# Performance work log

Measured on AMD Instinct MI355X. Metric: run time of the kernel, lower is better.

Reference implementation:

```python
import jax, jax.numpy as jnp
import numpy as np

B, T, U, D, INNER, VOCAB = 4, 256, 64, 512, 512, 2048

def setup_inputs() -> dict:
    key = jax.random.key(0)
    ks = jax.random.split(key, 6)
    return {
        "enc_state": jax.random.normal(ks[0], (B, T, D), jnp.float32),
        "dec_state": jax.random.normal(ks[1], (B, U, D), jnp.float32),
        "W1": jax.random.normal(ks[2], (2 * D, INNER), jnp.float32) * 0.02,
        "b1": jax.random.normal(ks[3], (INNER,), jnp.float32) * 0.02,
        "W2": jax.random.normal(ks[4], (INNER, VOCAB), jnp.float32) * 0.02,
        "b2": jax.random.normal(ks[5], (VOCAB,), jnp.float32) * 0.02,
    }

def reference(enc_state, dec_state, W1, b1, W2, b2):
    # concat([enc, dec]) @ W1 == enc @ W1[:D] + dec @ W1[D:]  (same math,
    # avoids materializing the [B,T,U,2D] repeat+cat tensor)
    d = enc_state.shape[-1]
    We, Wd = W1[:d], W1[d:]
    enc_proj = jnp.einsum('btd,dk->btk', enc_state, We)           # [B,T,INNER]
    dec_proj = jnp.einsum('bud,dk->buk', dec_state, Wd)           # [B,U,INNER]
    hidden = jnp.tanh(enc_proj[:, :, None, :] + dec_proj[:, None, :, :] + b1)  # [B,T,U,INNER]
    logits = jnp.einsum('btuk,kv->btuv', hidden, W2) + b2          # [B,T,U,VOCAB]
    return logits
```

## Files before the change

kernel.cpp:

```cpp
#include <hip/hip_runtime.h>
#include <hip/hip_bf16.h>

#define B_  4
#define T_  256
#define U_  64
#define D_  512
#define INNER_ 512
#define VOCAB_ 2048

typedef __attribute__((ext_vector_type(8))) short short8;
typedef __attribute__((ext_vector_type(4))) float f32x4;

__global__ __launch_bounds__(256) void prep_kernel(
    const float* __restrict__ enc, const float* __restrict__ dec,
    const float* __restrict__ W1, const float* __restrict__ b1,
    const float* __restrict__ W2,
    float* __restrict__ encP, float* __restrict__ decPb,
    __hip_bfloat16* __restrict__ W2T) {
  __shared__ float ldsbuf[16 * D_];
  int tid = threadIdx.x;
  int bidx = blockIdx.x;

  if (bidx < 320) {
    int ct = bidx & 3;
    int rt = bidx >> 2;
    const float* src; float* dst; int kOff; int addB1; int rowBase;
    if (rt < 64) { src = enc; dst = encP; kOff = 0; addB1 = 0; rowBase = rt * 16; }
    else { src = dec; dst = decPb; kOff = D_; addB1 = 1; rowBase = (rt - 64) * 16; }

    float (*As)[D_] = (float(*)[D_])ldsbuf;
    const float4* s4 = (const float4*)(src + (size_t)rowBase * D_);
    float4* a4 = (float4*)(&As[0][0]);
#pragma unroll
    for (int i = 0; i < 8; i++) a4[tid + 256 * i] = s4[tid + 256 * i];
    __syncthreads();

    int colQ = (tid & 31) * 4;
    int col = ct * 128 + colQ;
    int r0 = (tid >> 5) * 2;
    float a00=0,a01=0,a02=0,a03=0, a10=0,a11=0,a12=0,a13=0;
    const float* Wp = W1 + (size_t)kOff * INNER_ + col;
#pragma unroll 4
    for (int k = 0; k < D_; k++) {
      float4 w = *(const float4*)(Wp + (size_t)k * INNER_);
      float e0 = As[r0][k], e1 = As[r0 + 1][k];
      a00 += e0 * w.x; a01 += e0 * w.y; a02 += e0 * w.z; a03 += e0 * w.w;
      a10 += e1 * w.x; a11 += e1 * w.y; a12 += e1 * w.z; a13 += e1 * w.w;
    }
    float4 bb = {0,0,0,0};
    if (addB1) bb = *(const float4*)(b1 + col);
    float4 o0 = {a00 + bb.x, a01 + bb.y, a02 + bb.z, a03 + bb.w};
    float4 o1 = {a10 + bb.x, a11 + bb.y, a12 + bb.z, a13 + bb.w};
    *(float4*)(dst + (size_t)(rowBase + r0) * INNER_ + col) = o0;
    *(float4*)(dst + (size_t)(rowBase + r0 + 1) * INNER_ + col) = o1;
  } else {
    int b = bidx - 320;
    int vBase = (b & 63) * 32;
    int kBase = (b >> 6) * 32;
    float (*tile)[33] = (float(*)[33])ldsbuf;
    int tx = tid & 31, ty = tid >> 5;
#pragma unroll
    for (int i = 0; i < 32; i += 8)
      tile[ty + i][tx] = W2[(size_t)(kBase + ty + i) * VOCAB_ + vBase + tx];
    __syncthreads();
#pragma unroll
    for (int i = 0; i < 32; i += 8)
      W2T[(size_t)(vBase + ty + i) * INNER_ + kBase + tx] = __float2bfloat16(tile[tx][ty + i]);
  }
}

__global__ __launch_bounds__(256) void hidden_kernel(
    const float* __restrict__ encP, const float* __restrict__ decPb,
    __hip_bfloat16* __restrict__ H) {
  int gid = blockIdx.x * 256 + threadIdx.x;
  int k0 = (gid & 63) * 8;
  int r = gid >> 6;
  int u = r & 63;
  int bt = r >> 6;
  int b = bt >> 8;
  const float4* e = (const float4*)(encP + (size_t)bt * 512 + k0);
  const float4* dv = (const float4*)(decPb + (size_t)(b * 64 + u) * 512 + k0);
  float4 e0 = e[0], e1 = e[1];
  float4 d0 = dv[0], d1 = dv[1];
  union { __hip_bfloat16 h[8]; uint4 v; } p;
  p.h[0] = __float2bfloat16(tanhf(e0.x + d0.x));
  p.h[1] = __float2bfloat16(tanhf(e0.y + d0.y));
  p.h[2] = __float2bfloat16(tanhf(e0.z + d0.z));
  p.h[3] = __float2bfloat16(tanhf(e0.w + d0.w));
  p.h[4] = __float2bfloat16(tanhf(e1.x + d1.x));
  p.h[5] = __float2bfloat16(tanhf(e1.y + d1.y));
  p.h[6] = __float2bfloat16(tanhf(e1.z + d1.z));
  p.h[7] = __float2bfloat16(tanhf(e1.w + d1.w));
  *(uint4*)((__hip_bfloat16*)H + (size_t)r * 512 + k0) = p.v;
}

__device__ inline void gload_lds16(const void* g, void* l) {
  __builtin_amdgcn_global_load_lds(
      (const __attribute__((address_space(1))) unsigned int*)g,
      (__attribute__((address_space(3))) unsigned int*)l, 16, 0, 0);
}

__global__ __launch_bounds__(512, 1) void joint_gemm(
    const __hip_bfloat16* __restrict__ H, const __hip_bfloat16* __restrict__ W2T,
    const float* __restrict__ b2, float* __restrict__ out) {
  extern __shared__ char smem[];
  int tid = threadIdx.x;
  int lane = tid & 63, wave = tid >> 6;
  int wm = wave >> 2, wn = wave & 3;

  int bid = blockIdx.x;
  int wg = (bid & 7) * 256 + (bid >> 3);
  int rt = wg >> 3;
  int ct = wg & 7;
  size_t rowBase = (size_t)rt * 256;
  int colBase = ct * 256;

  int kswz = ((lane & 3) ^ ((lane >> 3) & 3)) * 8;
  int srow = wave * 16 + (lane >> 2);
  const __hip_bfloat16* pA = H   + (rowBase + srow) * 512 + kswz;
  const __hip_bfloat16* pB = W2T + (size_t)(colBase + srow) * 512 + kswz;
  char* ldsA = smem;
  char* ldsB = smem + 32768;

#define STAGE(t, buf) do {                                                    \
    const __hip_bfloat16* ga = pA + (size_t)(t) * 32;                         \
    const __hip_bfloat16* gb = pB + (size_t)(t) * 32;                         \
    char* la = ldsA + (buf) * 16384 + wave * 1024;                            \
    char* lb = ldsB + (buf) * 16384 + wave * 1024;                            \
    gload_lds16(ga,                 la);                                      \
    gload_lds16(ga + 128 * 512,     la + 8192);                               \
    gload_lds16(gb,                 lb);                                      \
    gload_lds16(gb + 128 * 512,     lb + 8192);                               \
  } while (0)

  int laneOff = (lane & 15) * 64 + (((lane >> 4) ^ (((lane & 15) >> 1) & 3)) * 16);
  int offA = wm * 8192 + laneOff;
  int offB = wn * 4096 + laneOff;

  float bv[4];
#pragma unroll
  for (int ni = 0; ni < 4; ni++) bv[ni] = b2[colBase + wn * 64 + ni * 16 + (lane & 15)];
  f32x4 acc[8][4];
#pragma unroll
  for (int mi = 0; mi < 8; mi++)
#pragma unroll
    for (int ni = 0; ni < 4; ni++)
      acc[mi][ni] = (f32x4){bv[ni], bv[ni], bv[ni], bv[ni]};

  asm volatile("s_waitcnt vmcnt(0)" ::: "memory");
  __builtin_amdgcn_sched_barrier(0);

  STAGE(0, 0);
  STAGE(1, 1);

#define KITER(t, buf, VMC, DOSTAGE) do {                                      \
    asm volatile("s_waitcnt vmcnt(" #VMC ")" ::: "memory");                   \
    __builtin_amdgcn_sched_barrier(0);                                        \
    __builtin_amdgcn_s_barrier();                                             \
    __builtin_amdgcn_sched_barrier(0);                                        \
    const char* baA = ldsA + (buf) * 16384;                                   \
    const char* baB = ldsB + (buf) * 16384;                                   \
    short8 afr[8], bfr[4];                                                    \
    _Pragma("unroll") for (int ni = 0; ni < 4; ni++)                          \
      bfr[ni] = *(const short8*)(baB + offB + ni * 1024);                     \
    _Pragma("unroll") for (int mi = 0; mi < 8; mi++)                          \
      afr[mi] = *(const short8*)(baA + offA + mi * 1024);                     \
    asm volatile("s_waitcnt lgkmcnt(0)" ::: "memory");                        \
    __builtin_amdgcn_sched_barrier(0);                                        \
    __builtin_amdgcn_s_barrier();                                             \
    __builtin_amdgcn_sched_barrier(0);                                        \
    if (DOSTAGE) { STAGE((t) + 2, (buf)); }                                   \
    __builtin_amdgcn_sched_barrier(0);                                        \
    __builtin_amdgcn_s_setprio(1);                                            \
    _Pragma("unroll") for (int mi = 0; mi < 8; mi++)                          \
      _Pragma("unroll") for (int ni = 0; ni < 4; ni++)                        \
        acc[mi][ni] = __builtin_amdgcn_mfma_f32_16x16x32_bf16(                \
            afr[mi], bfr[ni], acc[mi][ni], 0, 0, 0);                          \
    __builtin_amdgcn_s_setprio(0);                                            \
  } while (0)

#pragma unroll 2
  for (int t = 0; t < 14; ++t) KITER(t, (t & 1), 4, 1);
  KITER(14, 0, 4, 0);
  KITER(15, 1, 0, 0);
#undef KITER
#undef STAGE

  {
    float* lp = (float*)smem;
    float* outBase = out + rowBase * VOCAB_ + colBase;
#pragma unroll
    for (int r = 0; r < 4; r++) {
      __syncthreads();
      if (wm == (r >> 1)) {
        int mih = (r & 1) * 4;
#pragma unroll
        for (int q = 0; q < 4; q++) {
          int lrow0 = q * 16 + ((lane >> 4) << 2);
#pragma unroll
          for (int ni = 0; ni < 4; ni++) {
            int col = wn * 64 + ni * 16 + (lane & 15);
            f32x4 v = acc[mih + q][ni];
#pragma unroll
            for (int j = 0; j < 4; j++)
              lp[(lrow0 + j) * 260 + col] = v[j];
          }
        }
      }
      __syncthreads();
#pragma unroll
      for (int i = 0; i < 8; i++) {
        int c = tid + 512 * i;
        int row = c >> 6, cc = c & 63;
        f32x4 v = *(const f32x4*)(lp + row * 260 + cc * 4);
        __builtin_nontemporal_store(
            v, (f32x4*)(outBase + (size_t)(r * 64 + row) * VOCAB_ + cc * 4));
      }
    }
  }
}

extern "C" void kernel_launch(void* const* d_in, const int* in_sizes, int n_in,
                              void* d_out, int out_size, void* d_ws, size_t ws_size,
                              hipStream_t stream) {
  const float* enc = (const float*)d_in[0];
  const float* dec = (const float*)d_in[1];
  const float* W1  = (const float*)d_in[2];
  const float* b1  = (const float*)d_in[3];
  const float* W2  = (const float*)d_in[4];
  const float* b2  = (const float*)d_in[5];
  float* out = (float*)d_out;

  char* ws = (char*)d_ws;
  float* encP  = (float*)ws;
  float* decPb = (float*)(ws + (2u << 20));
  __hip_bfloat16* W2T = (__hip_bfloat16*)(ws + (2u << 20) + (512u << 10));
  __hip_bfloat16* H   = (__hip_bfloat16*)(ws + (2u << 20) + (512u << 10) + (2u << 20));

  static int smem_set = 0;
  if (!smem_set) {
    (void)hipFuncSetAttribute((const void*)joint_gemm,
                              hipFuncAttributeMaxDynamicSharedMemorySize, 66560);
    smem_set = 1;
  }

  prep_kernel<<<dim3(1344), 256, 0, stream>>>(enc, dec, W1, b1, W2, encP, decPb, W2T);
  hidden_kernel<<<16384, 256, 0, stream>>>(encP, decPb, H);
  joint_gemm<<<dim3(2048), 512, 66560, stream>>>(H, W2T, b2, out);
}
```

Baseline: 697.2 us.

## Double GEMM K-tile to 64 with wider LDS swizzle; grid-stride hidden kernel

The joint GEMM now stages a K-slice of 64 per iteration instead of 32. It uses 128 KB of double-buffered LDS with an 8-way XOR swizzle and does two fragment-load/MFMA halves per barrier pair, so the loop runs 8 iterations instead of 16. This halves the barrier and sync overhead per FLOP, at the cost of doubling LDS footprint. The hidden kernel becomes a grid-stride loop over 2048 blocks instead of 16384 blocks, to cut launch and scheduling overhead.

```diff
diff --git a/kernel.cpp b/kernel.cpp
--- a/kernel.cpp
+++ b/kernel.cpp
@@ -72,26 +72,27 @@
 __global__ __launch_bounds__(256) void hidden_kernel(
     const float* __restrict__ encP, const float* __restrict__ decPb,
     __hip_bfloat16* __restrict__ H) {
-  int gid = blockIdx.x * 256 + threadIdx.x;
-  int k0 = (gid & 63) * 8;
-  int r = gid >> 6;
-  int u = r & 63;
-  int bt = r >> 6;
-  int b = bt >> 8;
-  const float4* e = (const float4*)(encP + (size_t)bt * 512 + k0);
-  const float4* dv = (const float4*)(decPb + (size_t)(b * 64 + u) * 512 + k0);
-  float4 e0 = e[0], e1 = e[1];
-  float4 d0 = dv[0], d1 = dv[1];
-  union { __hip_bfloat16 h[8]; uint4 v; } p;
-  p.h[0] = __float2bfloat16(tanhf(e0.x + d0.x));
-  p.h[1] = __float2bfloat16(tanhf(e0.y + d0.y));
-  p.h[2] = __float2bfloat16(tanhf(e0.z + d0.z));
-  p.h[3] = __float2bfloat16(tanhf(e0.w + d0.w));
-  p.h[4] = __float2bfloat16(tanhf(e1.x + d1.x));
-  p.h[5] = __float2bfloat16(tanhf(e1.y + d1.y));
-  p.h[6] = __float2bfloat16(tanhf(e1.z + d1.z));
-  p.h[7] = __float2bfloat16(tanhf(e1.w + d1.w));
-  *(uint4*)((__hip_bfloat16*)H + (size_t)r * 512 + k0) = p.v;
+  for (int gid = blockIdx.x * 256 + threadIdx.x; gid < 4194304; gid += 2048 * 256) {
+    int k0 = (gid & 63) * 8;
+    int r = gid >> 6;
+    int u = r & 63;
+    int bt = r >> 6;
+    int b = bt >> 8;
+    const float4* e = (const float4*)(encP + (size_t)bt * 512 + k0);
+    const float4* dv = (const float4*)(decPb + (size_t)(b * 64 + u) * 512 + k0);
+    float4 e0 = e[0], e1 = e[1];
+    float4 d0 = dv[0], d1 = dv[1];
+    union { __hip_bfloat16 h[8]; uint4 v; } p;
+    p.h[0] = __float2bfloat16(tanhf(e0.x + d0.x));
+    p.h[1] = __float2bfloat16(tanhf(e0.y + d0.y));
+    p.h[2] = __float2bfloat16(tanhf(e0.z + d0.z));
+    p.h[3] = __float2bfloat16(tanhf(e0.w + d0.w));
+    p.h[4] = __float2bfloat16(tanhf(e1.x + d1.x));
+    p.h[5] = __float2bfloat16(tanhf(e1.y + d1.y));
+    p.h[6] = __float2bfloat16(tanhf(e1.z + d1.z));
+    p.h[7] = __float2bfloat16(tanhf(e1.w + d1.w));
+    *(uint4*)((__hip_bfloat16*)H + (size_t)r * 512 + k0) = p.v;
+  }
 }
 
 __device__ inline void gload_lds16(const void* g, void* l) {
@@ -115,27 +116,28 @@
   size_t rowBase = (size_t)rt * 256;
   int colBase = ct * 256;
 
-  int kswz = ((lane & 3) ^ ((lane >> 3) & 3)) * 8;
-  int srow = wave * 16 + (lane >> 2);
+  int kswz = ((tid & 7) ^ ((tid >> 3) & 7)) * 8;
+  int srow = tid >> 3;
   const __hip_bfloat16* pA = H   + (rowBase + srow) * 512 + kswz;
   const __hip_bfloat16* pB = W2T + (size_t)(colBase + srow) * 512 + kswz;
   char* ldsA = smem;
-  char* ldsB = smem + 32768;
+  char* ldsB = smem + 65536;
 
 #define STAGE(t, buf) do {                                                    \
-    const __hip_bfloat16* ga = pA + (size_t)(t) * 32;                         \
-    const __hip_bfloat16* gb = pB + (size_t)(t) * 32;                         \
-    char* la = ldsA + (buf) * 16384 + wave * 1024;                            \
-    char* lb = ldsB + (buf) * 16384 + wave * 1024;                            \
-    gload_lds16(ga,                 la);                                      \
-    gload_lds16(ga + 128 * 512,     la + 8192);                               \
-    gload_lds16(gb,                 lb);                                      \
-    gload_lds16(gb + 128 * 512,     lb + 8192);                               \
-  } while (0)
-
-  int laneOff = (lane & 15) * 64 + (((lane >> 4) ^ (((lane & 15) >> 1) & 3)) * 16);
-  int offA = wm * 8192 + laneOff;
-  int offB = wn * 4096 + laneOff;
+    const __hip_bfloat16* ga = pA + (size_t)(t) * 64;                         \
+    const __hip_bfloat16* gb = pB + (size_t)(t) * 64;                         \
+    char* la = ldsA + (buf) * 32768 + wave * 1024;                            \
+    char* lb = ldsB + (buf) * 32768 + wave * 1024;                            \
+    _Pragma("unroll")                                                         \
+    for (int j = 0; j < 4; j++) {                                             \
+      gload_lds16(ga + (size_t)j * 64 * 512, la + j * 8192);                  \
+      gload_lds16(gb + (size_t)j * 64 * 512, lb + j * 8192);                  \
+    } } while (0)
+
+  int lo0 = (lane & 15) * 128 + ((((lane >> 4)) ^ (lane & 7)) * 16);
+  int lo1 = (lane & 15) * 128 + (((4 + (lane >> 4)) ^ (lane & 7)) * 16);
+  int offA = wm * 16384;
+  int offB = wn * 8192;
 
   float bv[4];
 #pragma unroll
@@ -158,13 +160,25 @@
     __builtin_amdgcn_sched_barrier(0);                                        \
     __builtin_amdgcn_s_barrier();                                             \
     __builtin_amdgcn_sched_barrier(0);                                        \
-    const char* baA = ldsA + (buf) * 16384;                                   \
-    const char* baB = ldsB + (buf) * 16384;                                   \
+    const char* baA = ldsA + (buf) * 32768 + offA;                            \
+    const char* baB = ldsB + (buf) * 32768 + offB;                            \
     short8 afr[8], bfr[4];                                                    \
     _Pragma("unroll") for (int ni = 0; ni < 4; ni++)                          \
-      bfr[ni] = *(const short8*)(baB + offB + ni * 1024);                     \
-    _Pragma("unroll") for (int mi = 0; mi < 8; mi++)                          \
-      afr[mi] = *(const short8*)(baA + offA + mi * 1024);                     \
+      bfr[ni] = *(const short8*)(baB + ni * 2048 + lo0);                      \
+    _Pragma("unroll") for (int mi = 0; mi < 8; mi++)                          \
+      afr[mi] = *(const short8*)(baA + mi * 2048 + lo0);                      \
+    asm volatile("s_waitcnt lgkmcnt(0)" ::: "memory");                        \
+    __builtin_amdgcn_sched_barrier(0);                                        \
+    __builtin_amdgcn_s_setprio(1);                                            \
+    _Pragma("unroll") for (int mi = 0; mi < 8; mi++)                          \
+      _Pragma("unroll") for (int ni = 0; ni < 4; ni++)                        \
+        acc[mi][ni] = __builtin_amdgcn_mfma_f32_16x16x32_bf16(                \
+            afr[mi], bfr[ni], acc[mi][ni], 0, 0, 0);                          \
+    __builtin_amdgcn_s_setprio(0);                                            \
+    _Pragma("unroll") for (int ni = 0; ni < 4; ni++)                          \
+      bfr[ni] = *(const short8*)(baB + ni * 2048 + lo1);                      \
+    _Pragma("unroll") for (int mi = 0; mi < 8; mi++)                          \
+      afr[mi] = *(const short8*)(baA + mi * 2048 + lo1);                      \
     asm volatile("s_waitcnt lgkmcnt(0)" ::: "memory");                        \
     __builtin_amdgcn_sched_barrier(0);                                        \
     __builtin_amdgcn_s_barrier();                                             \
@@ -179,10 +193,10 @@
     __builtin_amdgcn_s_setprio(0);                                            \
   } while (0)
 
-#pragma unroll 2
-  for (int t = 0; t < 14; ++t) KITER(t, (t & 1), 4, 1);
-  KITER(14, 0, 4, 0);
-  KITER(15, 1, 0, 0);
+#pragma unroll
+  for (int t = 0; t < 6; ++t) KITER(t, (t & 1), 8, 1);
+  KITER(6, 0, 8, 0);
+  KITER(7, 1, 0, 0);
 #undef KITER
 #undef STAGE
 
@@ -240,11 +254,11 @@
   static int smem_set = 0;
   if (!smem_set) {
     (void)hipFuncSetAttribute((const void*)joint_gemm,
-                              hipFuncAttributeMaxDynamicSharedMemorySize, 66560);
+                              hipFuncAttributeMaxDynamicSharedMemorySize, 131072);
     smem_set = 1;
   }
 
   prep_kernel<<<dim3(1344), 256, 0, stream>>>(enc, dec, W1, b1, W2, encP, decPb, W2T);
-  hidden_kernel<<<16384, 256, 0, stream>>>(encP, decPb, H);
-  joint_gemm<<<dim3(2048), 512, 66560, stream>>>(H, W2T, b2, out);
-}
+  hidden_kernel<<<2048, 256, 0, stream>>>(encP, decPb, H);
+  joint_gemm<<<dim3(2048), 512, 131072, stream>>>(H, W2T, b2, out);
+}
```

Result: no change. 688.0 us (-1.3%).
